# Kernel tuning notes

Measured on AMD Instinct MI355X. Metric: run time of the kernel, lower is better.

## Reference

```python
import jax, jax.numpy as jnp
import numpy as np


def _apply_reflection(x, v):
    # Householder: x - 2 * v_hat * (v_hat . x), v_hat = v / ||v||
    v_norm_sq = jnp.sum(v * v, axis=-1, keepdims=True) + 1e-8
    v_hat = v / jnp.sqrt(v_norm_sq)
    vTx = jnp.sum(x * v_hat, axis=-1, keepdims=True)
    return x - 2.0 * v_hat * vTx


def setup_inputs() -> dict:
    key = jax.random.key(0)
    ks = jax.random.split(key, 7)
    B, S, d_model, rank = 4, 2048, 1024, 256
    n_expand, n_reflect = 16, 64
    x = jax.random.normal(ks[0], (B, S, rank), dtype=jnp.float32)
    Wr = jax.random.normal(ks[1], (n_reflect, rank), dtype=jnp.float32) / np.sqrt(rank)
    We = jax.random.normal(ks[2], (n_expand, rank), dtype=jnp.float32) / np.sqrt(rank)
    Wd = jax.random.normal(ks[3], (n_reflect, d_model), dtype=jnp.float32) / np.sqrt(d_model)
    expand_neurons = jax.random.normal(ks[4], (n_expand, rank, d_model), dtype=jnp.float32) / np.sqrt(rank)
    rr = jax.random.normal(ks[5], (n_reflect, rank), dtype=jnp.float32)
    reflect_r = rr / (jnp.linalg.norm(rr, axis=-1, keepdims=True) + 1e-8)
    rd = jax.random.normal(ks[6], (n_reflect, d_model), dtype=jnp.float32)
    reflect_d = rd / (jnp.linalg.norm(rd, axis=-1, keepdims=True) + 1e-8)
    return {"x": x, "Wr": Wr, "We": We, "Wd": Wd,
            "expand_neurons": expand_neurons, "reflect_r": reflect_r,
            "reflect_d": reflect_d, "reflect_k": 2}


def reference(x, Wr, We, Wd, expand_neurons, reflect_r, reflect_d, reflect_k):
    # --- latent reflections (top-k Householder in rank space) ---
    scores_r = jnp.einsum('bsr,nr->bsn', x, Wr)            # [B,S,n_reflect]
    _, indices_r = jax.lax.top_k(scores_r, reflect_k)      # [B,S,k]
    for i in range(reflect_k):
        v = reflect_r[indices_r[:, :, i]]                  # [B,S,rank]
        x = _apply_reflection(x, v)
    # --- soft expert combination over expand matrices ---
    scores_e = jnp.einsum('bsr,er->bse', x, We)            # [B,S,n_expand]
    weights_e = jax.nn.softmax(scores_e, axis=-1)
    # fused form of einsum('bsr,erd->bsed') followed by einsum('bsed,bse->bsd')
    x = jnp.einsum('bse,bsr,erd->bsd', weights_e, x, expand_neurons)  # [B,S,d_model]
    # --- output reflections (top-k Householder in d_model space) ---
    scores_d = jnp.einsum('bsd,nd->bsn', x, Wd)            # [B,S,n_reflect]
    _, indices_d = jax.lax.top_k(scores_d, reflect_k)
    for i in range(reflect_k):
        v = reflect_d[indices_d[:, :, i]]                  # [B,S,d_model]
        x = _apply_reflection(x, v)
    return (x, indices_r, weights_e, indices_d)
```

## Files before the change

### kernel.cpp

```cpp
#include <hip/hip_runtime.h>
#include <cmath>

#define TOK   8192
#define RNK   256
#define NEXP  16
#define NREF  64
#define DM    1024
#define KTOT  4096

#define Y_OFF  0
#define IR_OFF (TOK*DM)
#define W_OFF  (IR_OFF + TOK*2)
#define ID_OFF (W_OFF + TOK*NEXP)

#define EBT_BYTES ((size_t)DM * KTOT * 2)
#define XF_BYTES  ((size_t)TOK * RNK * 4)
#define XH_BYTES  ((size_t)TOK * RNK * 2)
#define GT_BYTES  ((size_t)NEXP * NREF * RNK * 2)
#define S_BYTES   ((size_t)TOK * NREF * 4)
#define G64_BYTES ((size_t)NREF * KTOT * 8)
#define SR_BYTES  ((size_t)TOK * NREF * 8)
#define WS_FULL   (EBT_BYTES + XF_BYTES + 2*XH_BYTES + 2*GT_BYTES + S_BYTES + G64_BYTES + SR_BYTES)

typedef __attribute__((ext_vector_type(8))) short short8;
typedef __attribute__((ext_vector_type(4))) float f32x4;
typedef const __attribute__((address_space(1))) void* gptr_t;
typedef __attribute__((address_space(3))) void* lptr_t;

__device__ inline unsigned short f2bf(float f) {
    unsigned int u = __float_as_uint(f);
    return (unsigned short)((u + 0x7fffu + ((u >> 16) & 1u)) >> 16);
}
__device__ inline float bf2f(unsigned short h) {
    return __uint_as_float(((unsigned int)h) << 16);
}
__device__ inline void split2(float v, unsigned short& h, unsigned short& l) {
    h = f2bf(v);
    l = f2bf(v - bf2f(h));
}
__device__ inline unsigned long long pack4(unsigned short a, unsigned short b,
                                           unsigned short c, unsigned short d) {
    return (unsigned long long)a | ((unsigned long long)b << 16)
         | ((unsigned long long)c << 32) | ((unsigned long long)d << 48);
}

__device__ inline void top2_64(double v, int idx, int& i0, int& i1) {
    double bv = v; int bi = idx;
    #pragma unroll
    for (int m = 1; m < 64; m <<= 1) {
        double ov = __shfl_xor(bv, m, 64);
        int    oi = __shfl_xor(bi, m, 64);
        if (ov > bv || (ov == bv && oi < bi)) { bv = ov; bi = oi; }
    }
    i0 = bi;
    double v2 = (idx == i0) ? -INFINITY : v;
    double bv2 = v2; int bi2 = idx;
    #pragma unroll
    for (int m = 1; m < 64; m <<= 1) {
        double ov = __shfl_xor(bv2, m, 64);
        int    oi = __shfl_xor(bi2, m, 64);
        if (ov > bv2 || (ov == bv2 && oi < bi2)) { bv2 = ov; bi2 = oi; }
    }
    i1 = bi2;
}

__global__ __launch_bounds__(256) void prep(
    const float* __restrict__ x, const float* __restrict__ Wr,
    const float* __restrict__ E, const float* __restrict__ Wd,
    double* __restrict__ Sr, unsigned short* __restrict__ Ebt,
    double* __restrict__ G64t,
    unsigned short* __restrict__ Gth, unsigned short* __restrict__ Gtl)
{
    __shared__ __align__(16) float lds_raw[64 * 68];
    const int bid = blockIdx.x;
    const int tid = threadIdx.x;
    const int w = tid >> 6, n = tid & 63;

    if (bid < 1024) {
        float* wt2 = lds_raw;
        const int t0 = bid * 8;
        double acc[2] = {0.0, 0.0};
        const float* xr0 = x + (size_t)(t0 + w * 2 + 0) * RNK;
        const float* xr1 = x + (size_t)(t0 + w * 2 + 1) * RNK;
        for (int d0 = 0; d0 < RNK; d0 += 64) {
            __syncthreads();
            #pragma unroll
            for (int rep = 0; rep < 4; ++rep) {
                int f = rep * 256 + tid;
                int nn = f >> 4, dgw = (f & 15) << 2;
                float4 v = *(const float4*)(Wr + (size_t)nn * RNK + d0 + dgw);
                *(float4*)&wt2[nn * 68 + dgw] = v;
            }
            __syncthreads();
            #pragma unroll
            for (int dg = 0; dg < 16; ++dg) {
                float4 e0 = *(const float4*)(xr0 + d0 + dg * 4);
                float4 e1 = *(const float4*)(xr1 + d0 + dg * 4);
                float4 w4 = *(const float4*)&wt2[n * 68 + dg * 4];
                #pragma unroll
                for (int j = 0; j < 4; ++j) {
                    double wv = (double)(&w4.x)[j];
                    acc[0] = fma((double)(&e0.x)[j], wv, acc[0]);
                    acc[1] = fma((double)(&e1.x)[j], wv, acc[1]);
                }
            }
        }
        #pragma unroll
        for (int i = 0; i < 2; ++i)
            Sr[(size_t)(t0 + w * 2 + i) * NREF + n] = acc[i];
    } else if (bid < 2048) {
        const int id = bid - 1024;
        const int k0 = (id & 63) * 64, d0 = (id >> 6) * 64;
        #pragma unroll
        for (int rep = 0; rep < 4; ++rep) {
            int idx = rep * 256 + tid;
            int r = idx >> 4, c4 = (idx & 15) << 2;
            float4 v = *(const float4*)(E + (size_t)(k0 + r) * DM + d0 + c4);
            lds_raw[r * 68 + c4 + 0] = v.x; lds_raw[r * 68 + c4 + 1] = v.y;
            lds_raw[r * 68 + c4 + 2] = v.z; lds_raw[r * 68 + c4 + 3] = v.w;
        }
        __syncthreads();
        #pragma unroll
        for (int rep = 0; rep < 4; ++rep) {
            int idx = rep * 256 + tid;
            int dr = idx >> 4, kc4 = (idx & 15) << 2;
            *(unsigned long long*)&Ebt[(size_t)(d0 + dr) * KTOT + k0 + kc4] =
                pack4(f2bf(lds_raw[(kc4 + 0) * 68 + dr]),
                      f2bf(lds_raw[(kc4 + 1) * 68 + dr]),
                      f2bf(lds_raw[(kc4 + 2) * 68 + dr]),
                      f2bf(lds_raw[(kc4 + 3) * 68 + dr]));
        }
    } else {
        float* wt2 = lds_raw;
        const int k = (bid - 2048) * 4 + w;
        double acc = 0.0;
        const float* erow = E + (size_t)k * DM;
        for (int d0 = 0; d0 < DM; d0 += 64) {
            __syncthreads();
            #pragma unroll
            for (int rep = 0; rep < 4; ++rep) {
                int f = rep * 256 + tid;
                int nn = f >> 4, dgw = (f & 15) << 2;
                float4 v = *(const float4*)(Wd + (size_t)nn * DM + d0 + dgw);
                *(float4*)&wt2[nn * 68 + dgw] = v;
            }
            __syncthreads();
            #pragma unroll
            for (int dg = 0; dg < 16; ++dg) {
                float4 e0 = *(const float4*)(erow + d0 + dg * 4);
                float4 w4 = *(const float4*)&wt2[n * 68 + dg * 4];
                #pragma unroll
                for (int j = 0; j < 4; ++j)
                    acc = fma((double)(&e0.x)[j], (double)(&w4.x)[j], acc);
            }
        }
        G64t[(size_t)n * KTOT + k] = acc;
        float gf = (float)acc;
        unsigned short h, lo;
        split2(gf, h, lo);
        const int e = k >> 8, r = k & 255;
        Gth[((size_t)(e * NREF + n)) * RNK + r] = h;
        Gtl[((size_t)(e * NREF + n)) * RNK + r] = lo;
    }
}

__global__ __launch_bounds__(512, 4) void k1s(
    const double* __restrict__ Sr, const float* __restrict__ x,
    const float* __restrict__ We, const float* __restrict__ reflect_r,
    const unsigned short* __restrict__ Gth, const unsigned short* __restrict__ Gtl,
    const double* __restrict__ G64t,
    float* __restrict__ xprime,
    unsigned short* __restrict__ Xh, unsigned short* __restrict__ Xl,
    float* __restrict__ out_ir, float* __restrict__ out_w,
    float* __restrict__ out_id)
{
    __shared__ __align__(16) char smem_u[16640];
    __shared__ float xs[16][260];
    __shared__ float wsh[16][16];
    __shared__ float sfin[16][64];
    float* we_lds = (float*)smem_u;
    float* red    = (float*)smem_u;

    const int tid = threadIdx.x;
    const int w = tid >> 6, lane = tid & 63;
    const int t0 = blockIdx.x * 16;

    #pragma unroll
    for (int rep = 0; rep < 2; ++rep) {
        int f = rep * 512 + tid;
        int row = f >> 6, c4 = (f & 63) << 2;
        float4 v = *(const float4*)(We + (size_t)row * RNK + c4);
        *(float4*)&we_lds[row * 260 + c4] = v;
    }
    __syncthreads();

    for (int it = 0; it < 2; ++it) {
        const int tloc = it * 8 + w;
        const int t = t0 + tloc;

        float4 xv = *(const float4*)(x + (size_t)t * RNK + lane * 4);
        double s = Sr[(size_t)t * NREF + lane];
        int i0, i1;
        top2_64(s, lane, i0, i1);

        #pragma unroll
        for (int rr = 0; rr < 2; ++rr) {
            int idx = rr ? i1 : i0;
            float4 vv = *(const float4*)(reflect_r + (size_t)idx * RNK + lane * 4);
            float sv = vv.x * xv.x + vv.y * xv.y + vv.z * xv.z + vv.w * xv.w;
            float vn = vv.x * vv.x + vv.y * vv.y + vv.z * vv.z + vv.w * vv.w;
            #pragma unroll
            for (int m = 1; m < 64; m <<= 1) {
                sv += __shfl_xor(sv, m, 64);
                vn += __shfl_xor(vn, m, 64);
            }
            float coef = 2.0f * sv / (vn + 1e-8f);
            xv.x -= coef * vv.x; xv.y -= coef * vv.y;
            xv.z -= coef * vv.z; xv.w -= coef * vv.w;
        }

        *(float4*)&xs[tloc][lane * 4] = xv;
        *(float4*)(xprime + (size_t)t * RNK + lane * 4) = xv;

        const int n16 = lane & 15;
        double se = 0.0;
        {
            const float* werow = &we_lds[n16 * 260];
            #pragma unroll 8
            for (int r4 = 0; r4 < RNK / 4; ++r4) {
                float4 xr = *(const float4*)(&xs[tloc][r4 * 4]);
                float4 wf = *(const float4*)(werow + r4 * 4);
                se += (double)xr.x * wf.x + (double)xr.y * wf.y
                    + (double)xr.z * wf.z + (double)xr.w * wf.w;
            }
        }
        float sef = (float)se;
        float mx = sef;
        #pragma unroll
        for (int m = 1; m < 16; m <<= 1) mx = fmaxf(mx, __shfl_xor(mx, m, 64));
        float ex = expf(sef - mx);
        float sm = ex;
        #pragma unroll
        for (int m = 1; m < 16; m <<= 1) sm += __shfl_xor(sm, m, 64);
        float wgt = ex / sm;

        if (lane < NEXP) {
            out_w[(size_t)t * NEXP + lane] = wgt;
            wsh[tloc][lane] = wgt;
        }
        if (lane == 0) {
            out_ir[(size_t)t * 2 + 0] = (float)i0;
            out_ir[(size_t)t * 2 + 1] = (float)i1;
        }

        unsigned short hx, lx, hy, ly, hz, lz, hw, lw;
        split2(xv.x, hx, lx); split2(xv.y, hy, ly);
        split2(xv.z, hz, lz); split2(xv.w, hw, lw);
        *(unsigned long long*)&Xh[(size_t)t * RNK + lane * 4] = pack4(hx, hy, hz, hw);
        *(unsigned long long*)&Xl[(size_t)t * RNK + lane * 4] = pack4(lx, ly, lz, lw);
    }
    __syncthreads();

    const int l = lane;
    short8 ah[8], al[8];
    {
        const size_t abase = (size_t)(t0 + (l & 15)) * RNK + (l >> 4) * 8;
        #pragma unroll
        for (int ks = 0; ks < 8; ++ks) {
            ah[ks] = *(const short8*)&Xh[abase + ks * 32];
            al[ks] = *(const short8*)&Xl[abase + ks * 32];
        }
    }

    f32x4 Sacc[4] = {};
    #pragma unroll
    for (int ei = 0; ei < 2; ++ei) {
        const int e = w * 2 + ei;
        f32x4 acc[4] = {};
        #pragma unroll
        for (int ks = 0; ks < 8; ++ks) {
            #pragma unroll
            for (int nn = 0; nn < 4; ++nn) {
                size_t gbase = ((size_t)(e * NREF + nn * 16 + (l & 15))) * RNK
                             + ks * 32 + (l >> 4) * 8;
                short8 bh = *(const short8*)&Gth[gbase];
                short8 bl = *(const short8*)&Gtl[gbase];
                acc[nn] = __builtin_amdgcn_mfma_f32_16x16x32_bf16(al[ks], bh, acc[nn], 0, 0, 0);
                acc[nn] = __builtin_amdgcn_mfma_f32_16x16x32_bf16(ah[ks], bl, acc[nn], 0, 0, 0);
                acc[nn] = __builtin_amdgcn_mfma_f32_16x16x32_bf16(ah[ks], bh, acc[nn], 0, 0, 0);
            }
        }
        #pragma unroll
        for (int j = 0; j < 4; ++j) {
            float wv = wsh[(l >> 4) * 4 + j][e];
            #pragma unroll
            for (int nn = 0; nn < 4; ++nn) Sacc[nn][j] += wv * acc[nn][j];
        }
    }
    if (w < 4) {
        #pragma unroll
        for (int nn = 0; nn < 4; ++nn)
            #pragma unroll
            for (int j = 0; j < 4; ++j)
                red[(w * 16 + (l >> 4) * 4 + j) * 64 + nn * 16 + (l & 15)] = Sacc[nn][j];
    }
    __syncthreads();
    if (w >= 4) {
        #pragma unroll
        for (int nn = 0; nn < 4; ++nn)
            #pragma unroll
            for (int j = 0; j < 4; ++j)
                red[((w - 4) * 16 + (l >> 4) * 4 + j) * 64 + nn * 16 + (l & 15)] += Sacc[nn][j];
    }
    __syncthreads();
    for (int i = tid; i < 16 * 64; i += 512) {
        int tt = i >> 6, nn = i & 63;
        float sv = red[(0 * 16 + tt) * 64 + nn] + red[(1 * 16 + tt) * 64 + nn]
                 + red[(2 * 16 + tt) * 64 + nn] + red[(3 * 16 + tt) * 64 + nn];
        sfin[tt][nn] = sv;
    }
    __syncthreads();

    const float TAU = 1e-3f;
    for (int ti = 0; ti < 2; ++ti) {
        const int tloc = w * 2 + ti;
        const int t = t0 + tloc;

        float cur = sfin[tloc][lane];
        int cand[4];
        float sval[4];
        #pragma unroll
        for (int c = 0; c < 4; ++c) {
            float bv = cur; int bi = lane;
            #pragma unroll
            for (int m = 1; m < 64; m <<= 1) {
                float ov = __shfl_xor(bv, m, 64);
                int   oi = __shfl_xor(bi, m, 64);
                if (ov > bv || (ov == bv && oi < bi)) { bv = ov; bi = oi; }
            }
            cand[c] = bi; sval[c] = bv;
            if (lane == bi) cur = -INFINITY;
        }

        int si0, si1;
        if (sval[0] - sval[1] > TAU && sval[1] - sval[2] > TAU) {
            si0 = cand[0]; si1 = cand[1];
        } else {
            double rs[4];
            #pragma unroll
            for (int c = 0; c < 4; ++c) {
                const double* grow = G64t + (size_t)cand[c] * KTOT;
                double acc = 0.0;
                #pragma unroll 4
                for (int i = 0; i < 64; ++i) {
                    int k = i * 64 + lane;
                    double a = (double)wsh[tloc][k >> 8] * (double)xs[tloc][k & 255];
                    acc = fma(a, grow[k], acc);
                }
                #pragma unroll
                for (int m = 1; m < 64; m <<= 1) acc += __shfl_xor(acc, m, 64);
                rs[c] = acc;
            }
            int b0 = 0;
            #pragma unroll
            for (int c = 1; c < 4; ++c)
                if (rs[c] > rs[b0] || (rs[c] == rs[b0] && cand[c] < cand[b0])) b0 = c;
            int b1 = (b0 == 0) ? 1 : 0;
            #pragma unroll
            for (int c = 0; c < 4; ++c) {
                if (c == b0) continue;
                if (rs[c] > rs[b1] || (rs[c] == rs[b1] && cand[c] < cand[b1])) b1 = c;
            }
            si0 = cand[b0]; si1 = cand[b1];
        }
        if (lane == 0) {
            out_id[(size_t)t * 2 + 0] = (float)si0;
            out_id[(size_t)t * 2 + 1] = (float)si1;
        }
    }
}

__global__ __launch_bounds__(256) void k2_fused(
    const unsigned short* __restrict__ Xh,
    const unsigned short* __restrict__ Ebt,
    const float* __restrict__ wts,
    float* __restrict__ y)
{
    __shared__ unsigned short As[128 * 32];
    __shared__ unsigned short Bs[128 * 32];
    __shared__ float wt[NEXP * 132];
    const int tid = threadIdx.x;
    const int l = tid & 63, w = tid >> 6;
    const int wr = w >> 1, wc = w & 1;
    const int tm0 = blockIdx.y * 128, n0 = blockIdx.x * 128;
    const int lrow = l >> 2, s = l & 3, g = l >> 4;

    #pragma unroll
    for (int rep = 0; rep < 8; ++rep) {
        int f = rep * 256 + tid;
        int row = f >> 4, e = f & 15;
        wt[e * 132 + row] = wts[(size_t)(tm0 + row) * NEXP + e];
    }

    f32x4 acc[4][4] = {};

    for (int e = 0; e < NEXP; ++e) {
        f32x4 acc_e[4][4] = {};
        for (int kb8 = 0; kb8 < 8; ++kb8) {
            const int kb = e * 8 + kb8;
            __syncthreads();
            #pragma unroll
            for (int i = 0; i < 2; ++i) {
                int row = w * 32 + i * 16 + lrow;
                int sw = ((s ^ ((row >> 1) & 3)) << 4);
                const char* ga = (const char*)Xh
                    + ((size_t)(tm0 + row) * RNK + kb8 * 32) * 2 + sw;
                __builtin_amdgcn_global_load_lds((gptr_t)ga,
                    (lptr_t)&As[(w * 32 + i * 16) * 32], 16, 0, 0);
                const char* gb = (const char*)Ebt
                    + ((size_t)(n0 + row) * KTOT + kb * 32) * 2 + sw;
                __builtin_amdgcn_global_load_lds((gptr_t)gb,
                    (lptr_t)&Bs[(w * 32 + i * 16) * 32], 16, 0, 0);
            }
            __syncthreads();

            short8 af[4], bv[4];
            #pragma unroll
            for (int m = 0; m < 4; ++m) {
                int row = wr * 64 + m * 16 + (l & 15);
                af[m] = *(const short8*)&As[row * 32 + ((g ^ ((row >> 1) & 3)) << 3)];
            }
            #pragma unroll
            for (int nn = 0; nn < 4; ++nn) {
                int row = wc * 64 + nn * 16 + (l & 15);
                bv[nn] = *(const short8*)&Bs[row * 32 + ((g ^ ((row >> 1) & 3)) << 3)];
            }
            #pragma unroll
            for (int m = 0; m < 4; ++m)
                #pragma unroll
                for (int nn = 0; nn < 4; ++nn)
                    acc_e[m][nn] = __builtin_amdgcn_mfma_f32_16x16x32_bf16(
                        af[m], bv[nn], acc_e[m][nn], 0, 0, 0);
        }
        #pragma unroll
        for (int m = 0; m < 4; ++m) {
            int rowb = wr * 64 + m * 16 + (l >> 4) * 4;
            float4 wm = *(const float4*)&wt[e * 132 + rowb];
            #pragma unroll
            for (int nn = 0; nn < 4; ++nn) {
                #pragma unroll
                for (int j = 0; j < 4; ++j)
                    acc[m][nn][j] += (&wm.x)[j] * acc_e[m][nn][j];
            }
        }
    }

    #pragma unroll
    for (int m = 0; m < 4; ++m) {
        int rbase = tm0 + wr * 64 + m * 16 + (l >> 4) * 4;
        #pragma unroll
        for (int nn = 0; nn < 4; ++nn) {
            int c = n0 + wc * 64 + nn * 16 + (l & 15);
            #pragma unroll
            for (int j = 0; j < 4; ++j)
                y[(size_t)(rbase + j) * DM + c] = acc[m][nn][j];
        }
    }
}

__global__ __launch_bounds__(256) void k3_post(
    const float* __restrict__ out_id, const float* __restrict__ reflect_d,
    float* __restrict__ y)
{
    const int tid = threadIdx.x;
    const int w = tid >> 6, lane = tid & 63;
    const int t = blockIdx.x * 4 + w;

    float4 yv[4];
    #pragma unroll
    for (int c = 0; c < 4; ++c)
        yv[c] = *(const float4*)(y + (size_t)t * DM + lane * 16 + c * 4);

    const int i0 = (int)out_id[(size_t)t * 2 + 0];
    const int i1 = (int)out_id[(size_t)t * 2 + 1];

    #pragma unroll
    for (int rr = 0; rr < 2; ++rr) {
        int idx = rr ? i1 : i0;
        const float* vrow = reflect_d + (size_t)idx * DM + lane * 16;
        float sv = 0.f, vn = 0.f;
        float4 vv[4];
        #pragma unroll
        for (int c = 0; c < 4; ++c) {
            vv[c] = *(const float4*)(vrow + c * 4);
            sv += vv[c].x * yv[c].x + vv[c].y * yv[c].y
                + vv[c].z * yv[c].z + vv[c].w * yv[c].w;
            vn += vv[c].x * vv[c].x + vv[c].y * vv[c].y
                + vv[c].z * vv[c].z + vv[c].w * vv[c].w;
        }
        #pragma unroll
        for (int m = 1; m < 64; m <<= 1) {
            sv += __shfl_xor(sv, m, 64);
            vn += __shfl_xor(vn, m, 64);
        }
        float coef = 2.0f * sv / (vn + 1e-8f);
        #pragma unroll
        for (int c = 0; c < 4; ++c) {
            yv[c].x -= coef * vv[c].x; yv[c].y -= coef * vv[c].y;
            yv[c].z -= coef * vv[c].z; yv[c].w -= coef * vv[c].w;
        }
    }
    #pragma unroll
    for (int c = 0; c < 4; ++c)
        *(float4*)(y + (size_t)t * DM + lane * 16 + c * 4) = yv[c];
}

__global__ __launch_bounds__(256) void k1_tokens(
    const float* __restrict__ x, const float* __restrict__ Wr,
    const float* __restrict__ We, const float* __restrict__ reflect_r,
    float* __restrict__ xprime, float* __restrict__ out_ir,
    float* __restrict__ out_w)
{
    __shared__ float xs[4][RNK];
    const int tid = threadIdx.x;
    const int w = tid >> 6, lane = tid & 63;
    const int t = blockIdx.x * 4 + w;

    float4 xv = *(const float4*)(x + (size_t)t * RNK + lane * 4);
    *(float4*)(&xs[w][lane * 4]) = xv;
    __syncthreads();

    double s = 0.0;
    {
        const float* wrow = Wr + (size_t)lane * RNK;
        for (int r4 = 0; r4 < RNK / 4; ++r4) {
            float4 xr = *(const float4*)(&xs[w][r4 * 4]);
            float4 wr = *(const float4*)(wrow + r4 * 4);
            s += (double)xr.x * wr.x + (double)xr.y * wr.y
               + (double)xr.z * wr.z + (double)xr.w * wr.w;
        }
    }
    int i0, i1;
    top2_64(s, lane, i0, i1);

    #pragma unroll
    for (int rr = 0; rr < 2; ++rr) {
        int idx = rr ? i1 : i0;
        float4 vv = *(const float4*)(reflect_r + (size_t)idx * RNK + lane * 4);
        float sv = vv.x * xv.x + vv.y * xv.y + vv.z * xv.z + vv.w * xv.w;
        float vn = vv.x * vv.x + vv.y * vv.y + vv.z * vv.z + vv.w * vv.w;
        #pragma unroll
        for (int m = 1; m < 64; m <<= 1) {
            sv += __shfl_xor(sv, m, 64);
            vn += __shfl_xor(vn, m, 64);
        }
        float coef = 2.0f * sv / (vn + 1e-8f);
        xv.x -= coef * vv.x; xv.y -= coef * vv.y;
        xv.z -= coef * vv.z; xv.w -= coef * vv.w;
    }
    __syncthreads();
    *(float4*)(&xs[w][lane * 4]) = xv;
    __syncthreads();

    *(float4*)(xprime + (size_t)t * RNK + lane * 4) = xv;

    const int n = lane & 15;
    double se = 0.0;
    {
        const float* werow = We + (size_t)n * RNK;
        for (int r4 = 0; r4 < RNK / 4; ++r4) {
            float4 xr = *(const float4*)(&xs[w][r4 * 4]);
            float4 wf = *(const float4*)(werow + r4 * 4);
            se += (double)xr.x * wf.x + (double)xr.y * wf.y
                + (double)xr.z * wf.z + (double)xr.w * wf.w;
        }
    }
    float sef = (float)se;
    float mx = sef;
    #pragma unroll
    for (int m = 1; m < 16; m <<= 1) mx = fmaxf(mx, __shfl_xor(mx, m, 64));
    float ex = expf(sef - mx);
    float sm = ex;
    #pragma unroll
    for (int m = 1; m < 16; m <<= 1) sm += __shfl_xor(sm, m, 64);
    float wgt = ex / sm;

    if (lane < NEXP) out_w[(size_t)t * NEXP + lane] = wgt;
    if (lane == 0) {
        out_ir[(size_t)t * 2 + 0] = (float)i0;
        out_ir[(size_t)t * 2 + 1] = (float)i1;
    }
}

__global__ __launch_bounds__(256) void k2_gemm(
    const float* __restrict__ xp, const float* __restrict__ wts,
    const float* __restrict__ E, float* __restrict__ y)
{
    __shared__ float As[16][132];
    __shared__ float Bs[16][132];
    const int tid = threadIdx.x;
    const int bn = blockIdx.x, bm = blockIdx.y;
    const int tm0 = bm * 128, tn0 = bn * 128;
    const int ty = tid >> 4, tx = tid & 15;
    float acc[8][8] = {};
    for (int kb = 0; kb < KTOT / 16; ++kb) {
        const int e = kb >> 4;
        const int rbase = (kb & 15) << 4;
        const int kglob = kb << 4;
        __syncthreads();
        #pragma unroll
        for (int h = 0; h < 2; ++h) {
            int f = tid + h * 256;
            int m = f >> 2, k4 = (f & 3) << 2;
            int t = tm0 + m;
            float4 a = *(const float4*)(xp + (size_t)t * RNK + rbase + k4);
            float wv = wts[(size_t)t * NEXP + e];
            As[k4 + 0][m] = a.x * wv; As[k4 + 1][m] = a.y * wv;
            As[k4 + 2][m] = a.z * wv; As[k4 + 3][m] = a.w * wv;
        }
        #pragma unroll
        for (int h = 0; h < 2; ++h) {
            int f = tid + h * 256;
            int kk = f >> 5, d4 = (f & 31) << 2;
            float4 b = *(const float4*)(E + (size_t)(kglob + kk) * DM + tn0 + d4);
            *(float4*)(&Bs[kk][d4]) = b;
        }
        __syncthreads();
        #pragma unroll
        for (int kk = 0; kk < 16; ++kk) {
            float4 a0 = *(const float4*)(&As[kk][ty * 8]);
            float4 a1 = *(const float4*)(&As[kk][ty * 8 + 4]);
            float4 b0 = *(const float4*)(&Bs[kk][tx * 8]);
            float4 b1 = *(const float4*)(&Bs[kk][tx * 8 + 4]);
            float av[8] = {a0.x, a0.y, a0.z, a0.w, a1.x, a1.y, a1.z, a1.w};
            float bw[8] = {b0.x, b0.y, b0.z, b0.w, b1.x, b1.y, b1.z, b1.w};
            #pragma unroll
            for (int i = 0; i < 8; ++i)
                #pragma unroll
                for (int j = 0; j < 8; ++j)
                    acc[i][j] = fmaf(av[i], bw[j], acc[i][j]);
        }
    }
    #pragma unroll
    for (int i = 0; i < 8; ++i) {
        int t = tm0 + ty * 8 + i;
        float* yrow = y + (size_t)t * DM + tn0 + tx * 8;
        *(float4*)yrow       = make_float4(acc[i][0], acc[i][1], acc[i][2], acc[i][3]);
        *(float4*)(yrow + 4) = make_float4(acc[i][4], acc[i][5], acc[i][6], acc[i][7]);
    }
}

__global__ __launch_bounds__(256) void k3_full(
    const float* __restrict__ Wd, const float* __restrict__ reflect_d,
    float* __restrict__ y, float* __restrict__ out_id)
{
    __shared__ float ys[4][DM];
    __shared__ float wds[64][17];
    const int tid = threadIdx.x;
    const int w = tid >> 6, lane = tid & 63;
    const int t = blockIdx.x * 4 + w;

    float4 yv[4];
    #pragma unroll
    for (int c = 0; c < 4; ++c) {
        yv[c] = *(const float4*)(y + (size_t)t * DM + lane * 16 + c * 4);
        *(float4*)(&ys[w][lane * 16 + c * 4]) = yv[c];
    }
    double s = 0.0;
    for (int kb = 0; kb < DM / 16; ++kb) {
        __syncthreads();
        {
            int row = tid >> 2, c4 = (tid & 3) << 2;
            float4 wv = *(const float4*)(Wd + (size_t)row * DM + kb * 16 + c4);
            wds[row][c4 + 0] = wv.x; wds[row][c4 + 1] = wv.y;
            wds[row][c4 + 2] = wv.z; wds[row][c4 + 3] = wv.w;
        }
        __syncthreads();
        #pragma unroll
        for (int i = 0; i < 16; ++i)
            s += (double)ys[w][kb * 16 + i] * (double)wds[lane][i];
    }
    int i0, i1;
    top2_64(s, lane, i0, i1);
    #pragma unroll
    for (int rr = 0; rr < 2; ++rr) {
        int idx = rr ? i1 : i0;
        const float* vrow = reflect_d + (size_t)idx * DM + lane * 16;
        float sv = 0.f, vn = 0.f;
        float4 vv[4];
        #pragma unroll
        for (int c = 0; c < 4; ++c) {
            vv[c] = *(const float4*)(vrow + c * 4);
            sv += vv[c].x * yv[c].x + vv[c].y * yv[c].y
                + vv[c].z * yv[c].z + vv[c].w * yv[c].w;
            vn += vv[c].x * vv[c].x + vv[c].y * vv[c].y
                + vv[c].z * vv[c].z + vv[c].w * vv[c].w;
        }
        #pragma unroll
        for (int m = 1; m < 64; m <<= 1) {
            sv += __shfl_xor(sv, m, 64);
            vn += __shfl_xor(vn, m, 64);
        }
        float coef = 2.0f * sv / (vn + 1e-8f);
        #pragma unroll
        for (int c = 0; c < 4; ++c) {
            yv[c].x -= coef * vv[c].x; yv[c].y -= coef * vv[c].y;
            yv[c].z -= coef * vv[c].z; yv[c].w -= coef * vv[c].w;
        }
    }
    #pragma unroll
    for (int c = 0; c < 4; ++c)
        *(float4*)(y + (size_t)t * DM + lane * 16 + c * 4) = yv[c];
    if (lane == 0) {
        out_id[(size_t)t * 2 + 0] = (float)i0;
        out_id[(size_t)t * 2 + 1] = (float)i1;
    }
}

extern "C" void kernel_launch(void* const* d_in, const int* in_sizes, int n_in,
                              void* d_out, int out_size, void* d_ws, size_t ws_size,
                              hipStream_t stream) {
    const float* x  = (const float*)d_in[0];
    const float* Wr = (const float*)d_in[1];
    const float* We = (const float*)d_in[2];
    const float* Wd = (const float*)d_in[3];
    const float* E  = (const float*)d_in[4];
    const float* rr = (const float*)d_in[5];
    const float* rd = (const float*)d_in[6];

    float* out    = (float*)d_out;
    float* y      = out + Y_OFF;
    float* out_ir = out + IR_OFF;
    float* out_w  = out + W_OFF;
    float* out_id = out + ID_OFF;

    if (ws_size >= WS_FULL) {
        char* p = (char*)d_ws;
        unsigned short* Ebt = (unsigned short*)p;  p += EBT_BYTES;
        float*          Xf  = (float*)p;           p += XF_BYTES;
        unsigned short* Xh  = (unsigned short*)p;  p += XH_BYTES;
        unsigned short* Xl  = (unsigned short*)p;  p += XH_BYTES;
        unsigned short* Gth = (unsigned short*)p;  p += GT_BYTES;
        unsigned short* Gtl = (unsigned short*)p;  p += GT_BYTES;
        float*          Sb  = (float*)p;           p += S_BYTES;
        double*         G64 = (double*)p;          p += G64_BYTES;
        double*         Srb = (double*)p;
        (void)Sb;

        prep<<<3072, 256, 0, stream>>>(x, Wr, E, Wd, Srb, Ebt, G64, Gth, Gtl);
        k1s<<<TOK / 16, 512, 0, stream>>>(Srb, x, We, rr, Gth, Gtl, G64, Xf,
                                          Xh, Xl, out_ir, out_w, out_id);
        k2_fused<<<dim3(DM / 128, TOK / 128), 256, 0, stream>>>(Xh, Ebt, out_w, y);
        k3_post<<<TOK / 4, 256, 0, stream>>>(out_id, rd, y);
    } else {
        float* xprime = (float*)d_ws;
        k1_tokens<<<TOK / 4, 256, 0, stream>>>(x, Wr, We, rr, xprime,
                                               out_ir, out_w);
        k2_gemm<<<dim3(DM / 128, TOK / 128), 256, 0, stream>>>(xprime, out_w, E, y);
        k3_full<<<TOK / 4, 256, 0, stream>>>(Wd, rd, y, out_id);
    }
}
```

Before: 275.8 us.

## Split token preprocessing kernel into per-token reflection/softmax and MFMA score kernels

```diff
diff --git a/kernel.cpp b/kernel.cpp
--- a/kernel.cpp
+++ b/kernel.cpp
@@ -164,101 +164,118 @@
     }
 }
 
-__global__ __launch_bounds__(512, 4) void k1s(
+__global__ __launch_bounds__(256) void k1a(
     const double* __restrict__ Sr, const float* __restrict__ x,
     const float* __restrict__ We, const float* __restrict__ reflect_r,
+    float* __restrict__ xprime,
+    unsigned short* __restrict__ Xh, unsigned short* __restrict__ Xl,
+    float* __restrict__ out_ir, float* __restrict__ out_w)
+{
+    __shared__ float we_lds[16 * 260];
+    __shared__ float xs[4][260];
+    const int tid = threadIdx.x;
+    const int w = tid >> 6, lane = tid & 63;
+    const int t = blockIdx.x * 4 + w;
+
+    #pragma unroll
+    for (int rep = 0; rep < 4; ++rep) {
+        int f = rep * 256 + tid;
+        int row = f >> 6, c4 = (f & 63) << 2;
+        float4 v = *(const float4*)(We + (size_t)row * RNK + c4);
+        *(float4*)&we_lds[row * 260 + c4] = v;
+    }
+    __syncthreads();
+
+    float4 xv = *(const float4*)(x + (size_t)t * RNK + lane * 4);
+    double s = Sr[(size_t)t * NREF + lane];
+    int i0, i1;
+    top2_64(s, lane, i0, i1);
+
+    #pragma unroll
+    for (int rr = 0; rr < 2; ++rr) {
+        int idx = rr ? i1 : i0;
+        float4 vv = *(const float4*)(reflect_r + (size_t)idx * RNK + lane * 4);
+        float sv = vv.x * xv.x + vv.y * xv.y + vv.z * xv.z + vv.w * xv.w;
+        float vn = vv.x * vv.x + vv.y * vv.y + vv.z * vv.z + vv.w * vv.w;
+        #pragma unroll
+        for (int m = 1; m < 64; m <<= 1) {
+            sv += __shfl_xor(sv, m, 64);
+            vn += __shfl_xor(vn, m, 64);
+        }
+        float coef = 2.0f * sv / (vn + 1e-8f);
+        xv.x -= coef * vv.x; xv.y -= coef * vv.y;
+        xv.z -= coef * vv.z; xv.w -= coef * vv.w;
+    }
+
+    *(float4*)&xs[w][lane * 4] = xv;
+    *(float4*)(xprime + (size_t)t * RNK + lane * 4) = xv;
+
+    const int n16 = lane & 15;
+    double se = 0.0;
+    {
+        const float* werow = &we_lds[n16 * 260];
+        double s0 = 0.0, s1 = 0.0, s2 = 0.0, s3 = 0.0;
+        #pragma unroll 4
+        for (int r4 = 0; r4 < RNK / 4; r4 += 4) {
+            #pragma unroll
+            for (int u = 0; u < 4; ++u) {
+                float4 xr = *(const float4*)(&xs[w][(r4 + u) * 4]);
+                float4 wf = *(const float4*)(werow + (r4 + u) * 4);
+                double p = (double)xr.x * wf.x + (double)xr.y * wf.y
+                         + (double)xr.z * wf.z + (double)xr.w * wf.w;
+                if (u == 0) s0 += p; else if (u == 1) s1 += p;
+                else if (u == 2) s2 += p; else s3 += p;
+            }
+        }
+        se = (s0 + s1) + (s2 + s3);
+    }
+    float sef = (float)se;
+    float mx = sef;
+    #pragma unroll
+    for (int m = 1; m < 16; m <<= 1) mx = fmaxf(mx, __shfl_xor(mx, m, 64));
+    float ex = expf(sef - mx);
+    float sm = ex;
+    #pragma unroll
+    for (int m = 1; m < 16; m <<= 1) sm += __shfl_xor(sm, m, 64);
+    float wgt = ex / sm;
+
+    if (lane < NEXP) out_w[(size_t)t * NEXP + lane] = wgt;
+    if (lane == 0) {
+        out_ir[(size_t)t * 2 + 0] = (float)i0;
+        out_ir[(size_t)t * 2 + 1] = (float)i1;
+    }
+
+    unsigned short hx, lx, hy, ly, hz, lz, hw, lw;
+    split2(xv.x, hx, lx); split2(xv.y, hy, ly);
+    split2(xv.z, hz, lz); split2(xv.w, hw, lw);
+    *(unsigned long long*)&Xh[(size_t)t * RNK + lane * 4] = pack4(hx, hy, hz, hw);
+    *(unsigned long long*)&Xl[(size_t)t * RNK + lane * 4] = pack4(lx, ly, lz, lw);
+}
+
+__global__ __launch_bounds__(512, 4) void k1b(
+    const float* __restrict__ xprime, const float* __restrict__ out_w,
     const unsigned short* __restrict__ Gth, const unsigned short* __restrict__ Gtl,
     const double* __restrict__ G64t,
-    float* __restrict__ xprime,
-    unsigned short* __restrict__ Xh, unsigned short* __restrict__ Xl,
-    float* __restrict__ out_ir, float* __restrict__ out_w,
+    const unsigned short* __restrict__ Xh, const unsigned short* __restrict__ Xl,
     float* __restrict__ out_id)
 {
-    __shared__ __align__(16) char smem_u[16640];
+    __shared__ __align__(16) float red[4 * 16 * 64];
     __shared__ float xs[16][260];
     __shared__ float wsh[16][16];
     __shared__ float sfin[16][64];
-    float* we_lds = (float*)smem_u;
-    float* red    = (float*)smem_u;
-
     const int tid = threadIdx.x;
     const int w = tid >> 6, lane = tid & 63;
     const int t0 = blockIdx.x * 16;
 
     #pragma unroll
-    for (int rep = 0; rep < 2; ++rep) {
+    for (int rep = 0; rep < 8; ++rep) {
         int f = rep * 512 + tid;
-        int row = f >> 6, c4 = (f & 63) << 2;
-        float4 v = *(const float4*)(We + (size_t)row * RNK + c4);
-        *(float4*)&we_lds[row * 260 + c4] = v;
-    }
-    __syncthreads();
-
-    for (int it = 0; it < 2; ++it) {
-        const int tloc = it * 8 + w;
-        const int t = t0 + tloc;
-
-        float4 xv = *(const float4*)(x + (size_t)t * RNK + lane * 4);
-        double s = Sr[(size_t)t * NREF + lane];
-        int i0, i1;
-        top2_64(s, lane, i0, i1);
-
-        #pragma unroll
-        for (int rr = 0; rr < 2; ++rr) {
-            int idx = rr ? i1 : i0;
-            float4 vv = *(const float4*)(reflect_r + (size_t)idx * RNK + lane * 4);
-            float sv = vv.x * xv.x + vv.y * xv.y + vv.z * xv.z + vv.w * xv.w;
-            float vn = vv.x * vv.x + vv.y * vv.y + vv.z * vv.z + vv.w * vv.w;
-            #pragma unroll
-            for (int m = 1; m < 64; m <<= 1) {
-                sv += __shfl_xor(sv, m, 64);
-                vn += __shfl_xor(vn, m, 64);
-            }
-            float coef = 2.0f * sv / (vn + 1e-8f);
-            xv.x -= coef * vv.x; xv.y -= coef * vv.y;
-            xv.z -= coef * vv.z; xv.w -= coef * vv.w;
-        }
-
-        *(float4*)&xs[tloc][lane * 4] = xv;
-        *(float4*)(xprime + (size_t)t * RNK + lane * 4) = xv;
-
-        const int n16 = lane & 15;
-        double se = 0.0;
-        {
-            const float* werow = &we_lds[n16 * 260];
-            #pragma unroll 8
-            for (int r4 = 0; r4 < RNK / 4; ++r4) {
-                float4 xr = *(const float4*)(&xs[tloc][r4 * 4]);
-                float4 wf = *(const float4*)(werow + r4 * 4);
-                se += (double)xr.x * wf.x + (double)xr.y * wf.y
-                    + (double)xr.z * wf.z + (double)xr.w * wf.w;
-            }
-        }
-        float sef = (float)se;
-        float mx = sef;
-        #pragma unroll
-        for (int m = 1; m < 16; m <<= 1) mx = fmaxf(mx, __shfl_xor(mx, m, 64));
-        float ex = expf(sef - mx);
-        float sm = ex;
-        #pragma unroll
-        for (int m = 1; m < 16; m <<= 1) sm += __shfl_xor(sm, m, 64);
-        float wgt = ex / sm;
-
-        if (lane < NEXP) {
-            out_w[(size_t)t * NEXP + lane] = wgt;
-            wsh[tloc][lane] = wgt;
-        }
-        if (lane == 0) {
-            out_ir[(size_t)t * 2 + 0] = (float)i0;
-            out_ir[(size_t)t * 2 + 1] = (float)i1;
-        }
-
-        unsigned short hx, lx, hy, ly, hz, lz, hw, lw;
-        split2(xv.x, hx, lx); split2(xv.y, hy, ly);
-        split2(xv.z, hz, lz); split2(xv.w, hw, lw);
-        *(unsigned long long*)&Xh[(size_t)t * RNK + lane * 4] = pack4(hx, hy, hz, hw);
-        *(unsigned long long*)&Xl[(size_t)t * RNK + lane * 4] = pack4(lx, ly, lz, lw);
-    }
+        int tok = f >> 6, c4 = (f & 63) << 2;
+        *(float4*)&xs[tok][c4] =
+            *(const float4*)(xprime + (size_t)(t0 + tok) * RNK + c4);
+    }
+    if (tid < 256)
+        wsh[tid >> 4][tid & 15] = out_w[(size_t)(t0 + (tid >> 4)) * NEXP + (tid & 15)];
     __syncthreads();
 
     const int l = lane;
@@ -748,8 +765,10 @@
         (void)Sb;
 
         prep<<<3072, 256, 0, stream>>>(x, Wr, E, Wd, Srb, Ebt, G64, Gth, Gtl);
-        k1s<<<TOK / 16, 512, 0, stream>>>(Srb, x, We, rr, Gth, Gtl, G64, Xf,
-                                          Xh, Xl, out_ir, out_w, out_id);
+        k1a<<<TOK / 4, 256, 0, stream>>>(Srb, x, We, rr, Xf,
+                                         Xh, Xl, out_ir, out_w);
+        k1b<<<TOK / 16, 512, 0, stream>>>(Xf, out_w, Gth, Gtl, G64,
+                                          Xh, Xl, out_id);
         k2_fused<<<dim3(DM / 128, TOK / 128), 256, 0, stream>>>(Xh, Ebt, out_w, y);
         k3_post<<<TOK / 4, 256, 0, stream>>>(out_id, rd, y);
     } else {
```

Measured after the change: 289.4 us. 1.05x slower.
